# Kernel optimization log

Measured on AMD Instinct MI355X. Metric: run time of the kernel, lower is better.

The kernel has to match this reference:

```python
import jax, jax.numpy as jnp
import numpy as np

B, N, D_MODEL = 2, 2048, 1024
H, HEAD_DIM, D1 = 16, 128, 2048
NK, RANK = 16, 32
GAMMA = 0.999


def setup_inputs() -> dict:
    key = jax.random.key(0)
    ks = jax.random.split(key, 12)
    std = 0.02
    return {
        "x": jax.random.normal(ks[0], (B, N, D_MODEL), jnp.float32),
        "Wu": jax.random.normal(ks[1], (D_MODEL, D1), jnp.float32) * std,
        "bu": jax.random.normal(ks[2], (D1,), jnp.float32) * std,
        "Wv": jax.random.normal(ks[3], (D_MODEL, D1), jnp.float32) * std,
        "bv": jax.random.normal(ks[4], (D1,), jnp.float32) * std,
        "Wo": jax.random.normal(ks[5], (D1, D_MODEL), jnp.float32) * std,
        "bo": jax.random.normal(ks[6], (D_MODEL,), jnp.float32) * std,
        # SKI low-rank Toeplitz kernel factors at nk inducing relative positions
        "a_pos": jax.random.normal(ks[7], (H, NK, RANK), jnp.float32) * 0.1,
        "b_pos": jax.random.normal(ks[8], (H, RANK, HEAD_DIM), jnp.float32) * 0.1,
        "a_neg": jax.random.normal(ks[9], (H, NK, RANK), jnp.float32) * 0.1,
        "b_neg": jax.random.normal(ks[10], (H, RANK, HEAD_DIM), jnp.float32) * 0.1,
        "t_zero": jax.random.normal(ks[11], (H, HEAD_DIM), jnp.float32) * 0.1,
    }


def _interp_decay_kernel(a, b, n):
    # low-rank kernel at nk inducing points: [h, nk, d]
    k_ind = jnp.einsum("hkr,hrd->hkd", a, b)
    lags = jnp.arange(1, n)                      # lags 1..n-1
    p = (lags - 1.0) / (n - 2.0) * (NK - 1)      # map lag onto inducing grid
    lo = jnp.floor(p).astype(jnp.int32)
    hi = jnp.minimum(lo + 1, NK - 1)
    w = (p - lo)[None, :, None]
    k = k_ind[:, lo, :] * (1.0 - w) + k_ind[:, hi, :] * w  # [h, n-1, d]
    decay = (GAMMA ** lags)[None, :, None]
    return k * decay


def reference(x, Wu, bu, Wv, bv, Wo, bo, a_pos, b_pos, a_neg, b_neg, t_zero):
    u = jax.nn.silu(x @ Wu + bu)                 # [b, n, d1]
    v = jax.nn.silu(x @ Wv + bv)                 # [b, n, d1]
    n = v.shape[1]
    vh = v.reshape(v.shape[0], n, H, HEAD_DIM)   # [b, n, h, d]

    kp = _interp_decay_kernel(a_pos, b_pos, n)   # [h, n-1, d]
    kn = _interp_decay_kernel(a_neg, b_neg, n)   # [h, n-1, d]
    m = 2 * n
    k_full = jnp.zeros((H, m, HEAD_DIM), vh.dtype)
    k_full = k_full.at[:, 0].set(t_zero)
    k_full = k_full.at[:, 1:n].set(kp)
    k_full = k_full.at[:, m - jnp.arange(1, n)].set(kn)  # non-causal (negative lags)

    # circular FFT convolution along the sequence axis
    vf = jnp.fft.rfft(vh, n=m, axis=1)                    # [b, mf, h, d]
    kf = jnp.transpose(jnp.fft.rfft(k_full, axis=1), (1, 0, 2))[None]  # [1, mf, h, d]
    y = jnp.fft.irfft(vf * kf, n=m, axis=1)[:, :n]        # [b, n, h, d]

    out = u * y.reshape(y.shape[0], n, D1)                # elementwise gate
    return out @ Wo + bo
```

## Files before the change

kernel.cpp:

```cpp
#include <hip/hip_runtime.h>
#include <hip/hip_bf16.h>
#include <stdint.h>
#include <stddef.h>

#define BB 2
#define NSEQ 2048
#define DM 1024
#define H 16
#define HD 128
#define D1 2048
#define NKI 16
#define RANKI 32
#define MROWS (BB * NSEQ)
#define VPROWS 6144
#define NTAP 28
#define NPAIR 13
#define NCHUNK 128
#define CLEN 16
#define GAMMA_F 0.999f
#define G_CL 0.9841201f
#define LN_G (-1.00050033e-3f)

__device__ constexpr int TAPS[NTAP] = {
  1, 2, 138, 139, 274, 275, 411, 412, 547, 548, 684,
  820, 821, 956, 957, 1093, 1094, 1229, 1230, 1366,
  1502, 1503, 1638, 1639, 1775, 1776, 1911, 1912};
__device__ constexpr int LEADL[NPAIR] = {1, 138, 274, 411, 547, 820, 956, 1093, 1229, 1502, 1638, 1775, 1911};
__device__ constexpr int LEADI[NPAIR] = {0, 2, 4, 6, 8, 11, 13, 15, 17, 20, 22, 24, 26};
#define SGL0_L 684
#define SGL0_I 10
#define SGL1_L 1366
#define SGL1_I 19

typedef short short8 __attribute__((ext_vector_type(8)));
typedef float floatx4 __attribute__((ext_vector_type(4)));

__device__ __forceinline__ float bf2f(unsigned short u) {
  union { unsigned int i; float f; } v; v.i = ((unsigned int)u) << 16; return v.f;
}
__device__ __forceinline__ unsigned short f2bf(float f) {
  union { float f; unsigned int i; } v; v.f = f;
  unsigned int r = (v.i + 0x7FFFu + ((v.i >> 16) & 1u)) >> 16;
  return (unsigned short)r;
}
__device__ __forceinline__ float bflo(unsigned int p) {
  union { unsigned int i; float f; } v; v.i = p << 16; return v.f;
}
__device__ __forceinline__ float bfhi(unsigned int p) {
  union { unsigned int i; float f; } v; v.i = p & 0xffff0000u; return v.f;
}
__device__ __forceinline__ void async16(const unsigned short* g, unsigned short* l) {
  __builtin_amdgcn_global_load_lds(
      (const __attribute__((address_space(1))) unsigned int*)g,
      (__attribute__((address_space(3))) unsigned int*)l, 16, 0, 0);
}

#define CVT4 (MROWS * DM / 4)
__global__ __launch_bounds__(256) void prep_kernel(const float* __restrict__ x,
                                                   unsigned short* __restrict__ x_bf,
                                                   unsigned short* __restrict__ zrow) {
  int i = blockIdx.x * 256 + threadIdx.x;
  if (i < CVT4) {
    float4 f = ((const float4*)x)[i];
    ushort4 o;
    o.x = f2bf(f.x); o.y = f2bf(f.y); o.z = f2bf(f.z); o.w = f2bf(f.w);
    ((ushort4*)x_bf)[i] = o;
  } else {
    int j = i - CVT4;
    if (j < 256) {
      uint4 z; z.x = z.y = z.z = z.w = 0u;
      ((uint4*)zrow)[j] = z;
    }
  }
}

__device__ __forceinline__ float KinterpL(const float* kk, int l, int d) {
  if (l < 1) return 0.0f;
  float p = (float)(l - 1) * (15.0f / 2046.0f);
  int lo = (int)p; if (lo > 15) lo = 15;
  int hi = lo + 1; if (hi > 15) hi = 15;
  float w = p - (float)lo;
  float v = kk[lo * HD + d] * (1.0f - w) + kk[hi * HD + d] * w;
  return v * __powf(GAMMA_F, (float)l);
}

__global__ __launch_bounds__(256) void wprep_kernel(const float* __restrict__ Wu,
                                                    const float* __restrict__ Wv,
                                                    const float* __restrict__ Wo,
                                                    unsigned short* __restrict__ WT2,
                                                    unsigned short* __restrict__ WoT,
                                                    const float* __restrict__ ap,
                                                    const float* __restrict__ bp,
                                                    const float* __restrict__ an,
                                                    const float* __restrict__ bn,
                                                    float* __restrict__ dtp,
                                                    float* __restrict__ dtn) {
  int blk = blockIdx.x;
  int tid = threadIdx.x;
  if (blk < 6144) {
    __shared__ unsigned short t[32][33];
    const float* in; unsigned short* out;
    int rows, cols, bx, by;
    if (blk < 2048) {
      in = Wo; out = WoT; rows = D1; cols = DM;
      bx = (blk & 31) * 32; by = (blk >> 5) * 32;
    } else {
      int local = blk - 2048;
      int z = local >> 11, l2 = local & 2047;
      in = z ? Wv : Wu; out = WT2 + (size_t)z * D1 * DM;
      rows = DM; cols = D1;
      bx = (l2 & 63) * 32; by = (l2 >> 6) * 32;
    }
    int tx = tid & 31, ty = tid >> 5;
#pragma unroll
    for (int j = 0; j < 32; j += 8)
      t[ty + j][tx] = f2bf(in[(size_t)(by + ty + j) * cols + bx + tx]);
    __syncthreads();
#pragma unroll
    for (int j = 0; j < 32; j += 8)
      out[(size_t)(bx + ty + j) * rows + by + tx] = t[tx][ty + j];
  } else {
    __shared__ float kk[NKI * HD];
    int e0 = blk - 6144;
    int h = e0 & 15, dir = e0 >> 4;
    const float* a = (dir ? an : ap) + h * NKI * RANKI;
    const float* b = (dir ? bn : bp) + h * RANKI * HD;
    for (int e = tid; e < NKI * HD; e += 256) {
      int k = e >> 7, d = e & 127;
      float s = 0.0f;
#pragma unroll
      for (int r = 0; r < RANKI; ++r) s += a[k * RANKI + r] * b[r * HD + d];
      kk[e] = s;
    }
    __syncthreads();
    float* dt = (dir ? dtn : dtp) + (size_t)h * NTAP * HD;
    for (int e = tid; e < NTAP * HD; e += 256) {
      int j = e >> 7, d = e & 127;
      int l = TAPS[j];
      float K0 = KinterpL(kk, l, d);
      float K1 = KinterpL(kk, l - 1, d);
      float K2 = KinterpL(kk, l - 2, d);
      dt[e] = K0 - 2.0f * GAMMA_F * K1 + (GAMMA_F * GAMMA_F) * K2;
    }
  }
}

__global__ __launch_bounds__(512) void gemm_uv8(const unsigned short* __restrict__ A,
                                                const unsigned short* __restrict__ Bt,
                                                const float* __restrict__ bu,
                                                const float* __restrict__ bv,
                                                unsigned short* __restrict__ U,
                                                unsigned short* __restrict__ Vp) {
  __shared__ unsigned short lds[65536];
  constexpr int K = DM;
  constexpr int NT = K / 64;
  int lin = blockIdx.y * 16 + blockIdx.x;
  int swz = (lin & 7) * 32 + (lin >> 3);
  int n0 = (swz & 15) * 256;
  int m0 = (swz >> 4) * 256;
  int tid = threadIdx.x;
  int lane = tid & 63, w = tid >> 6;
  int wm = w >> 2, wn = w & 3;
  int q = lane >> 4, l16 = lane & 15;
  int srow = lane >> 3;
  int soff = ((lane & 7) ^ srow) << 3;
  const unsigned short* Ab = A + (size_t)(m0 + w * 8 + srow) * K + soff;
  const unsigned short* Bb = Bt + (size_t)(n0 + w * 8 + srow) * K + soff;
  unsigned aoff0 = w * 512;
  unsigned boff0 = 32768u + w * 512;
  int swk0 = (q ^ (l16 & 7)) << 3;
  int swk1 = ((4 | q) ^ (l16 & 7)) << 3;
  int pAr = wm * 8192;
  int pBr = 32768 + (wn >> 1) * 8192;
  int rB0 = (wn & 1) * 64;

  floatx4 acc[8][4];
#pragma unroll
  for (int f = 0; f < 8; ++f)
#pragma unroll
    for (int g = 0; g < 4; ++g) acc[f][g] = (floatx4){0.f, 0.f, 0.f, 0.f};

  auto stage = [&](int p, int t) {
    const unsigned short* a = Ab + t * 64;
    const unsigned short* b = Bb + t * 64;
    unsigned ao = aoff0 + p * 16384;
    unsigned bo = boff0 + p * 16384;
    async16(a,               &lds[ao]);
    async16(a + (size_t)64 * K,  &lds[ao + 4096]);
    async16(a + (size_t)128 * K, &lds[ao + 8192]);
    async16(a + (size_t)192 * K, &lds[ao + 12288]);
    async16(b,               &lds[bo]);
    async16(b + (size_t)64 * K,  &lds[bo + 4096]);
    async16(b + (size_t)128 * K, &lds[bo + 8192]);
    async16(b + (size_t)192 * K, &lds[bo + 12288]);
  };

  stage(0, 0);
  stage(1, 1);
  asm volatile("s_waitcnt vmcnt(8)" ::: "memory");
  __builtin_amdgcn_s_barrier();

  for (int t = 0; t < NT; ++t) {
    int p = t & 1;
    const unsigned short* As = &lds[pAr + p * 16384];
    const unsigned short* Bs = &lds[pBr + p * 16384];
#pragma unroll
    for (int mh = 0; mh < 2; ++mh) {
      short8 af[4][2], bfr[4][2];
#pragma unroll
      for (int f = 0; f < 4; ++f) {
        int rh = ((mh * 4 + f) * 16 + l16) * 64;
        af[f][0] = *(const short8*)(As + rh + swk0);
        af[f][1] = *(const short8*)(As + rh + swk1);
      }
#pragma unroll
      for (int g = 0; g < 4; ++g) {
        int rh = (rB0 + g * 16 + l16) * 64;
        bfr[g][0] = *(const short8*)(Bs + rh + swk0);
        bfr[g][1] = *(const short8*)(Bs + rh + swk1);
      }
      __builtin_amdgcn_s_setprio(1);
#pragma unroll
      for (int f = 0; f < 4; ++f)
#pragma unroll
        for (int g = 0; g < 4; ++g) {
          acc[mh * 4 + f][g] = __builtin_amdgcn_mfma_f32_16x16x32_bf16(
              af[f][0], bfr[g][0], acc[mh * 4 + f][g], 0, 0, 0);
          acc[mh * 4 + f][g] = __builtin_amdgcn_mfma_f32_16x16x32_bf16(
              af[f][1], bfr[g][1], acc[mh * 4 + f][g], 0, 0, 0);
        }
      __builtin_amdgcn_s_setprio(0);
    }
    if (t == NT - 1) break;
    asm volatile("" ::: "memory");
    __builtin_amdgcn_s_barrier();
    if (t + 2 < NT) {
      stage(p, t + 2);
      asm volatile("s_waitcnt vmcnt(8)" ::: "memory");
    } else {
      asm volatile("s_waitcnt vmcnt(0)" ::: "memory");
    }
    __builtin_amdgcn_s_barrier();
  }

  int isv = (n0 >= 2048);
  const float* bias = isv ? bv : bu;
#pragma unroll
  for (int f = 0; f < 8; ++f) {
#pragma unroll
    for (int g = 0; g < 4; ++g) {
      int n = n0 + wn * 64 + g * 16 + l16;
      int nc = isv ? (n - 2048) : n;
      float bsv = bias[nc];
#pragma unroll
      for (int r = 0; r < 4; ++r) {
        int m = m0 + wm * 128 + f * 16 + q * 4 + r;
        float val = acc[f][g][r] + bsv;
        val = val / (1.0f + __expf(-val));
        if (isv) {
          size_t mrow = (size_t)(2048 + m + ((m >> 11) << 12));
          Vp[mrow * 2048 + nc] = f2bf(val);
        } else {
          U[(size_t)m * 2048 + nc] = f2bf(val);
        }
      }
    }
  }
}

template <int MTILES, int KCH>
__global__ __launch_bounds__(256) void gemm_out(const unsigned short* __restrict__ A,
                                                const unsigned short* __restrict__ Bt,
                                                const float* __restrict__ bias,
                                                float* __restrict__ C,
                                                int M, int N, int K) {
  constexpr int AREG = MTILES * 1024;
  constexpr int BREG = 4096;
  __shared__ unsigned short Al[2][AREG * KCH];
  __shared__ unsigned short Bl[2][BREG * KCH];
  int m0 = blockIdx.y * (MTILES * 32), n0 = blockIdx.x * 128;
  int tid = threadIdx.x;
  int lane = tid & 63, w = tid >> 6;
  int rw = (w >> 1) * (MTILES * 16), cw = (w & 1) * 64;
  int q = lane >> 4, l16 = lane & 15;
  floatx4 acc[MTILES][4];
#pragma unroll
  for (int mt = 0; mt < MTILES; ++mt)
#pragma unroll
    for (int nt = 0; nt < 4; ++nt) acc[mt][nt] = (floatx4){0.f, 0.f, 0.f, 0.f};
  int grow = tid >> 2;
  int gcol = (tid & 3) * 8;
  const unsigned short* A0 = A + (size_t)(m0 + grow) * K + gcol;
  const unsigned short* A1 = A0 + (size_t)64 * K;
  const unsigned short* B0 = Bt + (size_t)(n0 + grow) * K + gcol;
  const unsigned short* B1 = B0 + (size_t)64 * K;
  int woff = w * 512;
  int nIter = K / (32 * KCH);
#pragma unroll
  for (int kc = 0; kc < KCH; ++kc) {
    async16(A0 + kc * 32, &Al[0][kc * AREG + woff]);
    if (MTILES == 4) async16(A1 + kc * 32, &Al[0][kc * AREG + 2048 + woff]);
    async16(B0 + kc * 32, &Bl[0][kc * BREG + woff]);
    async16(B1 + kc * 32, &Bl[0][kc * BREG + 2048 + woff]);
  }
  int p = 0;
  for (int i = 0; i < nIter; ++i) {
    __syncthreads();
    if (i + 1 < nIter) {
      int kn = (i + 1) * 32 * KCH;
#pragma unroll
      for (int kc = 0; kc < KCH; ++kc) {
        async16(A0 + kn + kc * 32, &Al[p ^ 1][kc * AREG + woff]);
        if (MTILES == 4) async16(A1 + kn + kc * 32, &Al[p ^ 1][kc * AREG + 2048 + woff]);
        async16(B0 + kn + kc * 32, &Bl[p ^ 1][kc * BREG + woff]);
        async16(B1 + kn + kc * 32, &Bl[p ^ 1][kc * BREG + 2048 + woff]);
      }
    }
#pragma unroll
    for (int kc = 0; kc < KCH; ++kc) {
      short8 af[MTILES], bfr[4];
#pragma unroll
      for (int i4 = 0; i4 < MTILES; ++i4)
        af[i4] = *(const short8*)(&Al[p][kc * AREG + (rw + i4 * 16 + l16) * 32 + q * 8]);
#pragma unroll
      for (int i4 = 0; i4 < 4; ++i4)
        bfr[i4] = *(const short8*)(&Bl[p][kc * BREG + (cw + i4 * 16 + l16) * 32 + q * 8]);
#pragma unroll
      for (int mt = 0; mt < MTILES; ++mt)
#pragma unroll
        for (int nt = 0; nt < 4; ++nt)
          acc[mt][nt] = __builtin_amdgcn_mfma_f32_16x16x32_bf16(af[mt], bfr[nt], acc[mt][nt], 0, 0, 0);
    }
    p ^= 1;
  }
#pragma unroll
  for (int mt = 0; mt < MTILES; ++mt) {
#pragma unroll
    for (int nt = 0; nt < 4; ++nt) {
      int n = n0 + cw + nt * 16 + l16;
      float bsv = bias[n];
#pragma unroll
      for (int r = 0; r < 4; ++r) {
        int m = m0 + rw + mt * 16 + q * 4 + r;
        C[(size_t)m * N + n] = acc[mt][nt][r] + bsv;
      }
    }
  }
}

__global__ __launch_bounds__(256, 1) void scan_chunks(const unsigned short* __restrict__ Vp,
                                                      const unsigned short* __restrict__ zr,
                                                      const float* __restrict__ dp,
                                                      const float* __restrict__ dn,
                                                      unsigned short* __restrict__ ypl,
                                                      unsigned short* __restrict__ ynl,
                                                      float* __restrict__ Sy_ex,
                                                      float* __restrict__ SG_ex) {
  int z = blockIdx.z;
  int dir = z >> 1, b = z & 1;
  int chunk = blockIdx.y;
  int c0 = blockIdx.x * 512 + threadIdx.x * 2;
  int h = c0 >> 7, d = c0 & 127;
  const float* dt = (dir ? dn : dp) + ((size_t)h * NTAP) * HD + d;
  float2 dreg[NTAP];
#pragma unroll
  for (int j = 0; j < NTAP; ++j) dreg[j] = *(const float2*)(dt + j * HD);
  const unsigned short* Vd = Vp + (size_t)b * VPROWS * D1 + (size_t)2048 * D1;
  unsigned short* yl = (dir ? ynl : ypl) + (size_t)b * NSEQ * D1 + c0;
  float sy0 = 0.f, sy1 = 0.f, sg0 = 0.f, sg1 = 0.f;
  float carry0[NPAIR], carry1[NPAIR];
  if (!dir) {
    int t0 = chunk * CLEN;
#pragma unroll
    for (int p = 0; p < NPAIR; ++p) {
      int tr = t0 - 1 - LEADL[p];
      const unsigned short* rb = (tr >= 0) ? (Vd + (size_t)tr * D1) : zr;
      unsigned int pk = *(const unsigned int*)(rb + c0);
      carry0[p] = bflo(pk); carry1[p] = bfhi(pk);
    }
    for (int i = 0; i < CLEN; ++i) {
      int t = t0 + i;
      float F0 = 0.f, F1 = 0.f;
#pragma unroll
      for (int p = 0; p < NPAIR; ++p) {
        int tr = t - LEADL[p];
        const unsigned short* rb = (tr >= 0) ? (Vd + (size_t)tr * D1) : zr;
        unsigned int pk = *(const unsigned int*)(rb + c0);
        float vl0 = bflo(pk), vl1 = bfhi(pk);
        F0 += dreg[LEADI[p]].x * vl0 + dreg[LEADI[p] + 1].x * carry0[p];
        F1 += dreg[LEADI[p]].y * vl1 + dreg[LEADI[p] + 1].y * carry1[p];
        carry0[p] = vl0; carry1[p] = vl1;
      }
      {
        int tr = t - SGL0_L;
        const unsigned short* rb = (tr >= 0) ? (Vd + (size_t)tr * D1) : zr;
        unsigned int pk = *(const unsigned int*)(rb + c0);
        F0 += dreg[SGL0_I].x * bflo(pk); F1 += dreg[SGL0_I].y * bfhi(pk);
      }
      {
        int tr = t - SGL1_L;
        const unsigned short* rb = (tr >= 0) ? (Vd + (size_t)tr * D1) : zr;
        unsigned int pk = *(const unsigned int*)(rb + c0);
        F0 += dreg[SGL1_I].x * bflo(pk); F1 += dreg[SGL1_I].y * bfhi(pk);
      }
      sg0 = GAMMA_F * sg0 + F0; sy0 = GAMMA_F * sy0 + sg0;
      sg1 = GAMMA_F * sg1 + F1; sy1 = GAMMA_F * sy1 + sg1;
      unsigned int pack = (unsigned int)f2bf(sy0) | ((unsigned int)f2bf(sy1) << 16);
      *(unsigned int*)(yl + (size_t)t * D1) = pack;
    }
  } else {
    int tstart = (NSEQ - 1) - chunk * CLEN;
#pragma unroll
    for (int p = 0; p < NPAIR; ++p) {
      int tr = tstart + 1 + LEADL[p];
      const unsigned short* rb = (tr <= NSEQ - 1) ? (Vd + (size_t)tr * D1) : zr;
      unsigned int pk = *(const unsigned int*)(rb + c0);
      carry0[p] = bflo(pk); carry1[p] = bfhi(pk);
    }
    for (int i = 0; i < CLEN; ++i) {
      int t = tstart - i;
      float F0 = 0.f, F1 = 0.f;
#pragma unroll
      for (int p = 0; p < NPAIR; ++p) {
        int tr = t + LEADL[p];
        const unsigned short* rb = (tr <= NSEQ - 1) ? (Vd + (size_t)tr * D1) : zr;
        unsigned int pk = *(const unsigned int*)(rb + c0);
        float vl0 = bflo(pk), vl1 = bfhi(pk);
        F0 += dreg[LEADI[p]].x * vl0 + dreg[LEADI[p] + 1].x * carry0[p];
        F1 += dreg[LEADI[p]].y * vl1 + dreg[LEADI[p] + 1].y * carry1[p];
        carry0[p] = vl0; carry1[p] = vl1;
      }
      {
        int tr = t + SGL0_L;
        const unsigned short* rb = (tr <= NSEQ - 1) ? (Vd + (size_t)tr * D1) : zr;
        unsigned int pk = *(const unsigned int*)(rb + c0);
        F0 += dreg[SGL0_I].x * bflo(pk); F1 += dreg[SGL0_I].y * bfhi(pk);
      }
      {
        int tr = t + SGL1_L;
        const unsigned short* rb = (tr <= NSEQ - 1) ? (Vd + (size_t)tr * D1) : zr;
        unsigned int pk = *(const unsigned int*)(rb + c0);
        F0 += dreg[SGL1_I].x * bflo(pk); F1 += dreg[SGL1_I].y * bfhi(pk);
      }
      sg0 = GAMMA_F * sg0 + F0; sy0 = GAMMA_F * sy0 + sg0;
      sg1 = GAMMA_F * sg1 + F1; sy1 = GAMMA_F * sy1 + sg1;
      unsigned int pack = (unsigned int)f2bf(sy0) | ((unsigned int)f2bf(sy1) << 16);
      *(unsigned int*)(yl + (size_t)t * D1) = pack;
    }
  }
  size_t sidx = ((size_t)z * NCHUNK + chunk) * D1 + c0;
  Sy_ex[sidx] = sy0; Sy_ex[sidx + 1] = sy1;
  SG_ex[sidx] = sg0; SG_ex[sidx + 1] = sg1;
}

__global__ __launch_bounds__(256) void state_scan(const float* __restrict__ Sy_ex,
                                                  const float* __restrict__ SG_ex,
                                                  float* __restrict__ Sy_in,
                                                  float* __restrict__ SG_in) {
  int idx = blockIdx.x * 256 + threadIdx.x;
  if (idx >= 4 * D1) return;
  int z = idx >> 11, c = idx & (D1 - 1);
  float ey = 0.f, eg = 0.f;
  for (int k = 0; k < NCHUNK; ++k) {
    size_t s = ((size_t)z * NCHUNK + k) * D1 + c;
    Sy_in[s] = ey; SG_in[s] = eg;
    float lex = Sy_ex[s], lgx = SG_ex[s];
    ey = lex + G_CL * (ey + (float)CLEN * eg);
    eg = lgx + G_CL * eg;
  }
}

__global__ __launch_bounds__(256) void combine_kernel(const unsigned short* __restrict__ ypl,
                                                      const unsigned short* __restrict__ ynl,
                                                      const unsigned short* __restrict__ Vp,
                                                      const float* __restrict__ Sy_in,
                                                      const float* __restrict__ SG_in,
                                                      const float* __restrict__ tz,
                                                      const unsigned short* __restrict__ U,
                                                      unsigned short* __restrict__ G) {
  int e = blockIdx.x * 256 + threadIdx.x;
  int cq = e & (D1 / 4 - 1);
  int c0 = cq * 4;
  int r = e >> 9;
  int t = r & (NSEQ - 1);
  int b = r >> 11;
  int kp = t >> 4;  float dpD = (float)((t & 15) + 1);
  int tau = (NSEQ - 1) - t;
  int kn = tau >> 4; float dnD = (float)((tau & 15) + 1);
  float gp = __expf(dpD * LN_G);
  float gn = __expf(dnD * LN_G);
  size_t ix = (size_t)r * D1 + c0;
  size_t sp = ((size_t)(b) * NCHUNK + kp) * D1 + c0;
  size_t sn = ((size_t)(2 + b) * NCHUNK + kn) * D1 + c0;
  uint2 pyl = *(const uint2*)(ypl + ix);
  uint2 pyn = *(const uint2*)(ynl + ix);
  uint2 pv  = *(const uint2*)(Vp + ((size_t)b * VPROWS + 2048 + t) * D1 + c0);
  uint2 pu  = *(const uint2*)(U + ix);
  float4 syp = *(const float4*)(Sy_in + sp);
  float4 sgp = *(const float4*)(SG_in + sp);
  float4 syn = *(const float4*)(Sy_in + sn);
  float4 sgn = *(const float4*)(SG_in + sn);
  float4 tzv = *(const float4*)(tz + c0);
  float yv[4], uv[4], vv[4];
  yv[0] = bflo(pyl.x) + gp * (syp.x + dpD * sgp.x) + bflo(pyn.x) + gn * (syn.x + dnD * sgn.x);
  yv[1] = bfhi(pyl.x) + gp * (syp.y + dpD * sgp.y) + bfhi(pyn.x) + gn * (syn.y + dnD * sgn.y);
  yv[2] = bflo(pyl.y) + gp * (syp.z + dpD * sgp.z) + bflo(pyn.y) + gn * (syn.z + dnD * sgn.z);
  yv[3] = bfhi(pyl.y) + gp * (syp.w + dpD * sgp.w) + bfhi(pyn.y) + gn * (syn.w + dnD * sgn.w);
  vv[0] = bflo(pv.x); vv[1] = bfhi(pv.x); vv[2] = bflo(pv.y); vv[3] = bfhi(pv.y);
  uv[0] = bflo(pu.x); uv[1] = bfhi(pu.x); uv[2] = bflo(pu.y); uv[3] = bfhi(pu.y);
  float tza[4] = {tzv.x, tzv.y, tzv.z, tzv.w};
  uint2 og;
  unsigned short g0 = f2bf(uv[0] * (yv[0] + tza[0] * vv[0]));
  unsigned short g1 = f2bf(uv[1] * (yv[1] + tza[1] * vv[1]));
  unsigned short g2 = f2bf(uv[2] * (yv[2] + tza[2] * vv[2]));
  unsigned short g3 = f2bf(uv[3] * (yv[3] + tza[3] * vv[3]));
  og.x = (unsigned int)g0 | ((unsigned int)g1 << 16);
  og.y = (unsigned int)g2 | ((unsigned int)g3 << 16);
  *(uint2*)(G + ix) = og;
}

extern "C" void kernel_launch(void* const* d_in, const int* in_sizes, int n_in,
                              void* d_out, int out_size, void* d_ws, size_t ws_size,
                              hipStream_t stream) {
  const float* x      = (const float*)d_in[0];
  const float* Wu     = (const float*)d_in[1];
  const float* bu     = (const float*)d_in[2];
  const float* Wv     = (const float*)d_in[3];
  const float* bv     = (const float*)d_in[4];
  const float* Wo     = (const float*)d_in[5];
  const float* bo     = (const float*)d_in[6];
  const float* a_pos  = (const float*)d_in[7];
  const float* b_pos  = (const float*)d_in[8];
  const float* a_neg  = (const float*)d_in[9];
  const float* b_neg  = (const float*)d_in[10];
  const float* t_zero = (const float*)d_in[11];
  float* out = (float*)d_out;

  char* ws = (char*)d_ws;
  unsigned short* x_bf  = (unsigned short*)ws; ws += (size_t)MROWS * DM * 2;
  unsigned short* u_ws  = (unsigned short*)ws; ws += (size_t)MROWS * D1 * 2;
  unsigned short* Vp    = (unsigned short*)ws; ws += (size_t)BB * VPROWS * D1 * 2;
  unsigned short* ypl   = (unsigned short*)ws; ws += (size_t)MROWS * D1 * 2;
  unsigned short* ynl   = (unsigned short*)ws; ws += (size_t)MROWS * D1 * 2;
  unsigned short* WoT   = (unsigned short*)ws; ws += (size_t)DM * D1 * 2;
  float* dtp   = (float*)ws; ws += (size_t)H * NTAP * HD * 4;
  float* dtn   = (float*)ws; ws += (size_t)H * NTAP * HD * 4;
  float* Sy_in = (float*)ws; ws += (size_t)4 * NCHUNK * D1 * 4;
  float* SG_in = (float*)ws; ws += (size_t)4 * NCHUNK * D1 * 4;
  unsigned short* zrow = (unsigned short*)ws; ws += (size_t)D1 * 2;
  float* Sy_ex = (float*)x_bf;
  float* SG_ex = (float*)x_bf + (size_t)4 * NCHUNK * D1;
  unsigned short* WT2 = ypl;

  dim3 tb256(256);
  prep_kernel<<<dim3(CVT4 / 256 + 1), tb256, 0, stream>>>(x, x_bf, zrow);
  wprep_kernel<<<dim3(6176), tb256, 0, stream>>>(
      Wu, Wv, Wo, WT2, WoT, a_pos, b_pos, a_neg, b_neg, dtp, dtn);
  gemm_uv8<<<dim3(16, 16), dim3(512), 0, stream>>>(x_bf, WT2, bu, bv, u_ws, Vp);
  scan_chunks<<<dim3(D1 / 512, NCHUNK, 4), tb256, 0, stream>>>(Vp, zrow, dtp, dtn, ypl, ynl, Sy_ex, SG_ex);
  state_scan<<<dim3((4 * D1 + 255) / 256), tb256, 0, stream>>>(Sy_ex, SG_ex, Sy_in, SG_in);
  combine_kernel<<<dim3((size_t)MROWS * D1 / 1024), tb256, 0, stream>>>(ypl, ynl, Vp, Sy_in, SG_in, t_zero, u_ws, u_ws);
  gemm_out<2, 2><<<dim3(DM / 128, MROWS / 64), tb256, 0, stream>>>(
      u_ws, WoT, bo, out, MROWS, DM, D1);
}
```

Baseline: 263.2 us.

## Double-buffer tap loads in chunk scan and hoist B fragment loads in GEMM

The chunked scan kernel now issues the global loads for the next time step into a second register buffer before consuming the current step. This lets memory latency overlap with the FMA recurrence instead of serialising load then compute each step. The GEMM main loop also loads the B-operand LDS fragments once per k-tile rather than once per M half. The costs are more live registers, which may reduce occupancy, and one extra redundant prefetch past the end of each chunk (clamped to zero rows or in-range rows).

```diff
diff --git a/kernel.cpp b/kernel.cpp
--- a/kernel.cpp
+++ b/kernel.cpp
@@ -15,6 +15,7 @@
 #define VPROWS 6144
 #define NTAP 28
 #define NPAIR 13
+#define NLOAD (NPAIR + 2)
 #define NCHUNK 128
 #define CLEN 16
 #define GAMMA_F 0.999f
@@ -204,20 +205,21 @@
     int p = t & 1;
     const unsigned short* As = &lds[pAr + p * 16384];
     const unsigned short* Bs = &lds[pBr + p * 16384];
+    short8 bfr[4][2];
+#pragma unroll
+    for (int g = 0; g < 4; ++g) {
+      int rh = (rB0 + g * 16 + l16) * 64;
+      bfr[g][0] = *(const short8*)(Bs + rh + swk0);
+      bfr[g][1] = *(const short8*)(Bs + rh + swk1);
+    }
 #pragma unroll
     for (int mh = 0; mh < 2; ++mh) {
-      short8 af[4][2], bfr[4][2];
+      short8 af[4][2];
 #pragma unroll
       for (int f = 0; f < 4; ++f) {
         int rh = ((mh * 4 + f) * 16 + l16) * 64;
         af[f][0] = *(const short8*)(As + rh + swk0);
         af[f][1] = *(const short8*)(As + rh + swk1);
-      }
-#pragma unroll
-      for (int g = 0; g < 4; ++g) {
-        int rh = (rB0 + g * 16 + l16) * 64;
-        bfr[g][0] = *(const short8*)(Bs + rh + swk0);
-        bfr[g][1] = *(const short8*)(Bs + rh + swk1);
       }
       __builtin_amdgcn_s_setprio(1);
 #pragma unroll
@@ -369,8 +371,42 @@
   unsigned short* yl = (dir ? ynl : ypl) + (size_t)b * NSEQ * D1 + c0;
   float sy0 = 0.f, sy1 = 0.f, sg0 = 0.f, sg1 = 0.f;
   float carry0[NPAIR], carry1[NPAIR];
+  unsigned int bufA[NLOAD], bufB[NLOAD];
+
   if (!dir) {
     int t0 = chunk * CLEN;
+    auto loadTaps = [&](unsigned int* buf, int t) {
+#pragma unroll
+      for (int p = 0; p < NPAIR; ++p) {
+        int tr = t - LEADL[p];
+        const unsigned short* rb = (tr >= 0) ? (Vd + (size_t)tr * D1) : zr;
+        buf[p] = *(const unsigned int*)(rb + c0);
+      }
+      {
+        int tr = t - SGL0_L;
+        buf[NPAIR] = *(const unsigned int*)(((tr >= 0) ? (Vd + (size_t)tr * D1) : zr) + c0);
+      }
+      {
+        int tr = t - SGL1_L;
+        buf[NPAIR + 1] = *(const unsigned int*)(((tr >= 0) ? (Vd + (size_t)tr * D1) : zr) + c0);
+      }
+    };
+    auto consume = [&](const unsigned int* buf, int t) {
+      float F0 = 0.f, F1 = 0.f;
+#pragma unroll
+      for (int p = 0; p < NPAIR; ++p) {
+        float vl0 = bflo(buf[p]), vl1 = bfhi(buf[p]);
+        F0 += dreg[LEADI[p]].x * vl0 + dreg[LEADI[p] + 1].x * carry0[p];
+        F1 += dreg[LEADI[p]].y * vl1 + dreg[LEADI[p] + 1].y * carry1[p];
+        carry0[p] = vl0; carry1[p] = vl1;
+      }
+      F0 += dreg[SGL0_I].x * bflo(buf[NPAIR]) + dreg[SGL1_I].x * bflo(buf[NPAIR + 1]);
+      F1 += dreg[SGL0_I].y * bfhi(buf[NPAIR]) + dreg[SGL1_I].y * bfhi(buf[NPAIR + 1]);
+      sg0 = GAMMA_F * sg0 + F0; sy0 = GAMMA_F * sy0 + sg0;
+      sg1 = GAMMA_F * sg1 + F1; sy1 = GAMMA_F * sy1 + sg1;
+      *(unsigned int*)(yl + (size_t)t * D1) =
+          (unsigned int)f2bf(sy0) | ((unsigned int)f2bf(sy1) << 16);
+    };
 #pragma unroll
     for (int p = 0; p < NPAIR; ++p) {
       int tr = t0 - 1 - LEADL[p];
@@ -378,38 +414,47 @@
       unsigned int pk = *(const unsigned int*)(rb + c0);
       carry0[p] = bflo(pk); carry1[p] = bfhi(pk);
     }
-    for (int i = 0; i < CLEN; ++i) {
-      int t = t0 + i;
+    loadTaps(bufA, t0);
+    for (int i = 0; i < CLEN; i += 2) {
+      loadTaps(bufB, t0 + i + 1);
+      consume(bufA, t0 + i);
+      loadTaps(bufA, t0 + i + 2);
+      consume(bufB, t0 + i + 1);
+    }
+  } else {
+    int tstart = (NSEQ - 1) - chunk * CLEN;
+    auto loadTaps = [&](unsigned int* buf, int t) {
+#pragma unroll
+      for (int p = 0; p < NPAIR; ++p) {
+        int tr = t + LEADL[p];
+        const unsigned short* rb = (tr <= NSEQ - 1) ? (Vd + (size_t)tr * D1) : zr;
+        buf[p] = *(const unsigned int*)(rb + c0);
+      }
+      {
+        int tr = t + SGL0_L;
+        buf[NPAIR] = *(const unsigned int*)(((tr <= NSEQ - 1) ? (Vd + (size_t)tr * D1) : zr) + c0);
+      }
+      {
+        int tr = t + SGL1_L;
+        buf[NPAIR + 1] = *(const unsigned int*)(((tr <= NSEQ - 1) ? (Vd + (size_t)tr * D1) : zr) + c0);
+      }
+    };
+    auto consume = [&](const unsigned int* buf, int t) {
       float F0 = 0.f, F1 = 0.f;
 #pragma unroll
       for (int p = 0; p < NPAIR; ++p) {
-        int tr = t - LEADL[p];
-        const unsigned short* rb = (tr >= 0) ? (Vd + (size_t)tr * D1) : zr;
-        unsigned int pk = *(const unsigned int*)(rb + c0);
-        float vl0 = bflo(pk), vl1 = bfhi(pk);
+        float vl0 = bflo(buf[p]), vl1 = bfhi(buf[p]);
         F0 += dreg[LEADI[p]].x * vl0 + dreg[LEADI[p] + 1].x * carry0[p];
         F1 += dreg[LEADI[p]].y * vl1 + dreg[LEADI[p] + 1].y * carry1[p];
         carry0[p] = vl0; carry1[p] = vl1;
       }
-      {
-        int tr = t - SGL0_L;
-        const unsigned short* rb = (tr >= 0) ? (Vd + (size_t)tr * D1) : zr;
-        unsigned int pk = *(const unsigned int*)(rb + c0);
-        F0 += dreg[SGL0_I].x * bflo(pk); F1 += dreg[SGL0_I].y * bfhi(pk);
-      }
-      {
-        int tr = t - SGL1_L;
-        const unsigned short* rb = (tr >= 0) ? (Vd + (size_t)tr * D1) : zr;
-        unsigned int pk = *(const unsigned int*)(rb + c0);
-        F0 += dreg[SGL1_I].x * bflo(pk); F1 += dreg[SGL1_I].y * bfhi(pk);
-      }
+      F0 += dreg[SGL0_I].x * bflo(buf[NPAIR]) + dreg[SGL1_I].x * bflo(buf[NPAIR + 1]);
+      F1 += dreg[SGL0_I].y * bfhi(buf[NPAIR]) + dreg[SGL1_I].y * bfhi(buf[NPAIR + 1]);
       sg0 = GAMMA_F * sg0 + F0; sy0 = GAMMA_F * sy0 + sg0;
       sg1 = GAMMA_F * sg1 + F1; sy1 = GAMMA_F * sy1 + sg1;
-      unsigned int pack = (unsigned int)f2bf(sy0) | ((unsigned int)f2bf(sy1) << 16);
-      *(unsigned int*)(yl + (size_t)t * D1) = pack;
-    }
-  } else {
-    int tstart = (NSEQ - 1) - chunk * CLEN;
+      *(unsigned int*)(yl + (size_t)t * D1) =
+          (unsigned int)f2bf(sy0) | ((unsigned int)f2bf(sy1) << 16);
+    };
 #pragma unroll
     for (int p = 0; p < NPAIR; ++p) {
       int tr = tstart + 1 + LEADL[p];
@@ -417,35 +462,12 @@
       unsigned int pk = *(const unsigned int*)(rb + c0);
       carry0[p] = bflo(pk); carry1[p] = bfhi(pk);
     }
-    for (int i = 0; i < CLEN; ++i) {
-      int t = tstart - i;
-      float F0 = 0.f, F1 = 0.f;
-#pragma unroll
-      for (int p = 0; p < NPAIR; ++p) {
-        int tr = t + LEADL[p];
-        const unsigned short* rb = (tr <= NSEQ - 1) ? (Vd + (size_t)tr * D1) : zr;
-        unsigned int pk = *(const unsigned int*)(rb + c0);
-        float vl0 = bflo(pk), vl1 = bfhi(pk);
-        F0 += dreg[LEADI[p]].x * vl0 + dreg[LEADI[p] + 1].x * carry0[p];
-        F1 += dreg[LEADI[p]].y * vl1 + dreg[LEADI[p] + 1].y * carry1[p];
-        carry0[p] = vl0; carry1[p] = vl1;
-      }
-      {
-        int tr = t + SGL0_L;
-        const unsigned short* rb = (tr <= NSEQ - 1) ? (Vd + (size_t)tr * D1) : zr;
-        unsigned int pk = *(const unsigned int*)(rb + c0);
-        F0 += dreg[SGL0_I].x * bflo(pk); F1 += dreg[SGL0_I].y * bfhi(pk);
-      }
-      {
-        int tr = t + SGL1_L;
-        const unsigned short* rb = (tr <= NSEQ - 1) ? (Vd + (size_t)tr * D1) : zr;
-        unsigned int pk = *(const unsigned int*)(rb + c0);
-        F0 += dreg[SGL1_I].x * bflo(pk); F1 += dreg[SGL1_I].y * bfhi(pk);
-      }
-      sg0 = GAMMA_F * sg0 + F0; sy0 = GAMMA_F * sy0 + sg0;
-      sg1 = GAMMA_F * sg1 + F1; sy1 = GAMMA_F * sy1 + sg1;
-      unsigned int pack = (unsigned int)f2bf(sy0) | ((unsigned int)f2bf(sy1) << 16);
-      *(unsigned int*)(yl + (size_t)t * D1) = pack;
+    loadTaps(bufA, tstart);
+    for (int i = 0; i < CLEN; i += 2) {
+      loadTaps(bufB, tstart - i - 1);
+      consume(bufA, tstart - i);
+      loadTaps(bufA, tstart - i - 2);
+      consume(bufB, tstart - i - 1);
     }
   }
   size_t sidx = ((size_t)z * NCHUNK + chunk) * D1 + c0;
```

New measurement: 280.4 us. +6.5%, slower.

## Replace output GEMM with 128x128 swizzled-LDS 512-thread kernel, hoist B fragment loads

Applied to the files above, without the earlier changes.

The output projection GEMM moves from a 64x128 tile with 256 threads and a K=64 double buffer to a 128x128 tile with 512 threads. It uses XOR-swizzled LDS, async global-to-LDS staging two tiles ahead, and a block-index swizzle meant to improve L2 locality. Bigger tiles raise operand reuse and cut global traffic, while the swizzle is meant to avoid LDS bank conflicts. In the uv GEMM, B fragments are now loaded once per k-step instead of once per M half, which cuts redundant LDS reads at the cost of holding more registers. The new output GEMM launches only 256 blocks, which could leave compute units underused.

```diff
diff --git a/kernel.cpp b/kernel.cpp
--- a/kernel.cpp
+++ b/kernel.cpp
@@ -204,20 +204,21 @@
     int p = t & 1;
     const unsigned short* As = &lds[pAr + p * 16384];
     const unsigned short* Bs = &lds[pBr + p * 16384];
+    short8 bfr[4][2];
+#pragma unroll
+    for (int g = 0; g < 4; ++g) {
+      int rh = (rB0 + g * 16 + l16) * 64;
+      bfr[g][0] = *(const short8*)(Bs + rh + swk0);
+      bfr[g][1] = *(const short8*)(Bs + rh + swk1);
+    }
 #pragma unroll
     for (int mh = 0; mh < 2; ++mh) {
-      short8 af[4][2], bfr[4][2];
+      short8 af[4][2];
 #pragma unroll
       for (int f = 0; f < 4; ++f) {
         int rh = ((mh * 4 + f) * 16 + l16) * 64;
         af[f][0] = *(const short8*)(As + rh + swk0);
         af[f][1] = *(const short8*)(As + rh + swk1);
-      }
-#pragma unroll
-      for (int g = 0; g < 4; ++g) {
-        int rh = (rB0 + g * 16 + l16) * 64;
-        bfr[g][0] = *(const short8*)(Bs + rh + swk0);
-        bfr[g][1] = *(const short8*)(Bs + rh + swk1);
       }
       __builtin_amdgcn_s_setprio(1);
 #pragma unroll
@@ -268,81 +269,102 @@
   }
 }
 
-template <int MTILES, int KCH>
-__global__ __launch_bounds__(256) void gemm_out(const unsigned short* __restrict__ A,
-                                                const unsigned short* __restrict__ Bt,
-                                                const float* __restrict__ bias,
-                                                float* __restrict__ C,
-                                                int M, int N, int K) {
-  constexpr int AREG = MTILES * 1024;
-  constexpr int BREG = 4096;
-  __shared__ unsigned short Al[2][AREG * KCH];
-  __shared__ unsigned short Bl[2][BREG * KCH];
-  int m0 = blockIdx.y * (MTILES * 32), n0 = blockIdx.x * 128;
+__global__ __launch_bounds__(512) void gemm_out2(const unsigned short* __restrict__ A,
+                                                 const unsigned short* __restrict__ Bt,
+                                                 const float* __restrict__ bias,
+                                                 float* __restrict__ C) {
+  __shared__ unsigned short lds[32768];
+  constexpr int K = D1;
+  constexpr int NT = K / 64;
+  int lin = blockIdx.y * 8 + blockIdx.x;
+  int swz = (lin & 7) * 32 + (lin >> 3);
+  int n0 = (swz & 7) * 128;
+  int m0 = (swz >> 3) * 128;
   int tid = threadIdx.x;
   int lane = tid & 63, w = tid >> 6;
-  int rw = (w >> 1) * (MTILES * 16), cw = (w & 1) * 64;
+  int wm = w >> 1, wn = w & 1;
   int q = lane >> 4, l16 = lane & 15;
-  floatx4 acc[MTILES][4];
-#pragma unroll
-  for (int mt = 0; mt < MTILES; ++mt)
-#pragma unroll
-    for (int nt = 0; nt < 4; ++nt) acc[mt][nt] = (floatx4){0.f, 0.f, 0.f, 0.f};
-  int grow = tid >> 2;
-  int gcol = (tid & 3) * 8;
-  const unsigned short* A0 = A + (size_t)(m0 + grow) * K + gcol;
-  const unsigned short* A1 = A0 + (size_t)64 * K;
-  const unsigned short* B0 = Bt + (size_t)(n0 + grow) * K + gcol;
-  const unsigned short* B1 = B0 + (size_t)64 * K;
-  int woff = w * 512;
-  int nIter = K / (32 * KCH);
-#pragma unroll
-  for (int kc = 0; kc < KCH; ++kc) {
-    async16(A0 + kc * 32, &Al[0][kc * AREG + woff]);
-    if (MTILES == 4) async16(A1 + kc * 32, &Al[0][kc * AREG + 2048 + woff]);
-    async16(B0 + kc * 32, &Bl[0][kc * BREG + woff]);
-    async16(B1 + kc * 32, &Bl[0][kc * BREG + 2048 + woff]);
-  }
-  int p = 0;
-  for (int i = 0; i < nIter; ++i) {
-    __syncthreads();
-    if (i + 1 < nIter) {
-      int kn = (i + 1) * 32 * KCH;
-#pragma unroll
-      for (int kc = 0; kc < KCH; ++kc) {
-        async16(A0 + kn + kc * 32, &Al[p ^ 1][kc * AREG + woff]);
-        if (MTILES == 4) async16(A1 + kn + kc * 32, &Al[p ^ 1][kc * AREG + 2048 + woff]);
-        async16(B0 + kn + kc * 32, &Bl[p ^ 1][kc * BREG + woff]);
-        async16(B1 + kn + kc * 32, &Bl[p ^ 1][kc * BREG + 2048 + woff]);
-      }
-    }
-#pragma unroll
-    for (int kc = 0; kc < KCH; ++kc) {
-      short8 af[MTILES], bfr[4];
-#pragma unroll
-      for (int i4 = 0; i4 < MTILES; ++i4)
-        af[i4] = *(const short8*)(&Al[p][kc * AREG + (rw + i4 * 16 + l16) * 32 + q * 8]);
-#pragma unroll
-      for (int i4 = 0; i4 < 4; ++i4)
-        bfr[i4] = *(const short8*)(&Bl[p][kc * BREG + (cw + i4 * 16 + l16) * 32 + q * 8]);
-#pragma unroll
-      for (int mt = 0; mt < MTILES; ++mt)
-#pragma unroll
-        for (int nt = 0; nt < 4; ++nt)
-          acc[mt][nt] = __builtin_amdgcn_mfma_f32_16x16x32_bf16(af[mt], bfr[nt], acc[mt][nt], 0, 0, 0);
-    }
-    p ^= 1;
-  }
-#pragma unroll
-  for (int mt = 0; mt < MTILES; ++mt) {
-#pragma unroll
-    for (int nt = 0; nt < 4; ++nt) {
-      int n = n0 + cw + nt * 16 + l16;
+  int srow = lane >> 3;
+  int soff = ((lane & 7) ^ srow) << 3;
+  const unsigned short* Ab = A + (size_t)(m0 + w * 8 + srow) * K + soff;
+  const unsigned short* Bb = Bt + (size_t)(n0 + w * 8 + srow) * K + soff;
+  unsigned aoff0 = w * 512;
+  unsigned boff0 = 16384u + w * 512;
+  int swk0 = (q ^ (l16 & 7)) << 3;
+  int swk1 = ((4 | q) ^ (l16 & 7)) << 3;
+
+  floatx4 acc[2][4];
+#pragma unroll
+  for (int f = 0; f < 2; ++f)
+#pragma unroll
+    for (int g = 0; g < 4; ++g) acc[f][g] = (floatx4){0.f, 0.f, 0.f, 0.f};
+
+  auto stage = [&](int p, int t) {
+    const unsigned short* a = Ab + t * 64;
+    const unsigned short* b = Bb + t * 64;
+    unsigned ao = aoff0 + p * 8192;
+    unsigned bo = boff0 + p * 8192;
+    async16(a,                  &lds[ao]);
+    async16(a + (size_t)64 * K, &lds[ao + 4096]);
+    async16(b,                  &lds[bo]);
+    async16(b + (size_t)64 * K, &lds[bo + 4096]);
+  };
+
+  stage(0, 0);
+  stage(1, 1);
+  asm volatile("s_waitcnt vmcnt(4)" ::: "memory");
+  __builtin_amdgcn_s_barrier();
+
+  for (int t = 0; t < NT; ++t) {
+    int p = t & 1;
+    const unsigned short* As = &lds[p * 8192];
+    const unsigned short* Bs = &lds[16384 + p * 8192];
+    short8 af[2][2], bfr[4][2];
+#pragma unroll
+    for (int g = 0; g < 4; ++g) {
+      int rh = (wn * 64 + g * 16 + l16) * 64;
+      bfr[g][0] = *(const short8*)(Bs + rh + swk0);
+      bfr[g][1] = *(const short8*)(Bs + rh + swk1);
+    }
+#pragma unroll
+    for (int f = 0; f < 2; ++f) {
+      int rh = (wm * 32 + f * 16 + l16) * 64;
+      af[f][0] = *(const short8*)(As + rh + swk0);
+      af[f][1] = *(const short8*)(As + rh + swk1);
+    }
+    __builtin_amdgcn_s_setprio(1);
+#pragma unroll
+    for (int f = 0; f < 2; ++f)
+#pragma unroll
+      for (int g = 0; g < 4; ++g) {
+        acc[f][g] = __builtin_amdgcn_mfma_f32_16x16x32_bf16(
+            af[f][0], bfr[g][0], acc[f][g], 0, 0, 0);
+        acc[f][g] = __builtin_amdgcn_mfma_f32_16x16x32_bf16(
+            af[f][1], bfr[g][1], acc[f][g], 0, 0, 0);
+      }
+    __builtin_amdgcn_s_setprio(0);
+    if (t == NT - 1) break;
+    asm volatile("" ::: "memory");
+    __builtin_amdgcn_s_barrier();
+    if (t + 2 < NT) {
+      stage(p, t + 2);
+      asm volatile("s_waitcnt vmcnt(4)" ::: "memory");
+    } else {
+      asm volatile("s_waitcnt vmcnt(0)" ::: "memory");
+    }
+    __builtin_amdgcn_s_barrier();
+  }
+
+#pragma unroll
+  for (int f = 0; f < 2; ++f) {
+#pragma unroll
+    for (int g = 0; g < 4; ++g) {
+      int n = n0 + wn * 64 + g * 16 + l16;
       float bsv = bias[n];
 #pragma unroll
       for (int r = 0; r < 4; ++r) {
-        int m = m0 + rw + mt * 16 + q * 4 + r;
-        C[(size_t)m * N + n] = acc[mt][nt][r] + bsv;
+        int m = m0 + wm * 32 + f * 16 + q * 4 + r;
+        C[(size_t)m * DM + n] = acc[f][g][r] + bsv;
       }
     }
   }
@@ -560,6 +582,5 @@
   scan_chunks<<<dim3(D1 / 512, NCHUNK, 4), tb256, 0, stream>>>(Vp, zrow, dtp, dtn, ypl, ynl, Sy_ex, SG_ex);
   state_scan<<<dim3((4 * D1 + 255) / 256), tb256, 0, stream>>>(Sy_ex, SG_ex, Sy_in, SG_in);
   combine_kernel<<<dim3((size_t)MROWS * D1 / 1024), tb256, 0, stream>>>(ypl, ynl, Vp, Sy_in, SG_in, t_zero, u_ws, u_ws);
-  gemm_out<2, 2><<<dim3(DM / 128, MROWS / 64), tb256, 0, stream>>>(
-      u_ws, WoT, bo, out, MROWS, DM, D1);
-}
+  gemm_out2<<<dim3(8, 32), dim3(512), 0, stream>>>(u_ws, WoT, bo, out);
+}
```

Result: no change. 258.6 us (-1.8%).
